# Optimization experiments

Hardware: AMD Instinct MI355X
Metric: run time of the kernel (lower is better)

The kernel has to match this reference:

```python
import jax, jax.numpy as jnp
import numpy as np

N = 4096   # number of observations
Q = 1024   # number of spatial locations (dist_matrix side)


def setup_inputs() -> dict:
    key = jax.random.key(0)
    k1, k2, k3, k4 = jax.random.split(key, 4)
    y_true = jax.random.normal(k1, (N, 1), dtype=jnp.float32)
    y_pred = jax.random.normal(k2, (N, 1), dtype=jnp.float32)
    Z_idx = jax.random.randint(k3, (N, 1), 0, Q).astype(jnp.int64)
    # symmetric distance matrix from random 2D coordinates
    coords = jax.random.uniform(k4, (Q, 2), dtype=jnp.float32) * 10.0
    diff = coords[:, None, :] - coords[None, :, :]
    dist_matrix = jnp.sqrt(jnp.sum(diff * diff, axis=-1) + 1e-12)
    sig2e = jnp.asarray(1.0, dtype=jnp.float32)
    sig2bs = jnp.ones((2,), dtype=jnp.float32)
    return {"y_true": y_true, "y_pred": y_pred, "Z_idx": Z_idx,
            "dist_matrix": dist_matrix, "sig2e": sig2e, "sig2bs": sig2bs}


def reference(y_true, y_pred, Z_idx, dist_matrix, sig2e, sig2bs):
    # NLL for the 'spatial' mixed-effects mode (custom_loss_lm).
    # V = sig2e*I + Z D Z^T with Z the one-hot indicator of Z_idx and
    # D[a,b] = sig2bs[0]*exp(-dist[a,b]/(2*sig2bs[1])).
    # Z D Z^T for one-hot Z is simply the row/col gather D[idx][:, idx],
    # which avoids materializing the dense N x Q indicator matrix.
    n = y_true.shape[0]
    idx = Z_idx[:, 0]
    D = sig2bs[0] * jnp.exp(-dist_matrix / (2.0 * sig2bs[1]))   # (Q, Q)
    V = sig2e * jnp.eye(n, dtype=jnp.float32) + D[idx][:, idx]  # (N, N)
    r = y_true - y_pred                                          # (N, 1)
    V_inv_r = jnp.linalg.solve(V, r)                             # (N, 1)
    quad = jnp.sum(r * V_inv_r)
    _, logdet = jnp.linalg.slogdet(V)
    log2pi = jnp.asarray(np.log(2.0 * np.pi), dtype=jnp.float32)
    total_loss = 0.5 * n * log2pi + 0.5 * logdet + 0.5 * quad
    return total_loss
```

## Files before the change

kernel.cpp:

```cpp
#include <hip/hip_runtime.h>
#include <math.h>

#define NN 4096
#define QQ 1024
#define LDA 1032
#define AF (1025 * 1032)


__device__ __forceinline__ void potrf64_run(float (&x)[16], int i, int q,
                                            float2 (&col2)[2][64]) {
#pragma unroll
    for (int qk = 0; qk < 4; ++qk) {
#pragma unroll
        for (int c2 = 0; c2 < 8; ++c2) {
            const int k = qk * 16 + 2 * c2;
            const int ck = 2 * c2;
            const int b = c2 & 1;
            if (q == qk) {
                float xk = x[ck];
                float d0 = __shfl(xk, k, 64);
                float rs0 = rsqrtf(d0);
                float l0 = (i == k) ? d0 * rs0 : xk * rs0;
                if (i >= k) x[ck] = l0;
                float lk1 = __shfl(l0, k + 1, 64);
                float x1v = fmaf(-l0, lk1, x[ck + 1]);
                float d1 = __shfl(x1v, k + 1, 64);
                float rs1 = rsqrtf(d1);
                float l1 = (i == k + 1) ? d1 * rs1 : x1v * rs1;
                if (i >= k + 1) x[ck + 1] = l1;
                col2[b][i] = make_float2(l0, l1);
            }
            __syncthreads();
            if (16 * q + 15 > k + 1 && i > k) {
                float2 lp = col2[b][i];
                const float4* cp = (const float4*)(&col2[b][16 * q]);
#pragma unroll
                for (int m2 = 0; m2 < 8; ++m2) {
                    float4 v = cp[m2];
                    if (16 * q + 2 * m2 > k + 1)
                        x[2 * m2] = fmaf(-lp.x, v.x, fmaf(-lp.y, v.y, x[2 * m2]));
                    if (16 * q + 2 * m2 + 1 > k + 1)
                        x[2 * m2 + 1] = fmaf(-lp.x, v.z, fmaf(-lp.y, v.w, x[2 * m2 + 1]));
                }
            }
        }
    }
}

template<int K, int M>
struct TAcc {
    static __device__ __forceinline__ void run(const float (&Lb)[64][65], const float (&x)[64],
                                               float& a0, float& a1) {
        if constexpr (M < K)     a0 = fmaf(-Lb[K][M], x[M], a0);
        if constexpr (M + 1 < K) a1 = fmaf(-Lb[K][M + 1], x[M + 1], a1);
        if constexpr (M + 2 < K) TAcc<K, M + 2>::run(Lb, x, a0, a1);
    }
};
template<int K>
struct TStep {
    static __device__ __forceinline__ void run(const float (&Lb)[64][65], const float (&dinv)[64],
                                               float (&x)[64]) {
        if constexpr (K < 64) {
            float a0 = x[K], a1 = 0.f;
            TAcc<K, 0>::run(Lb, x, a0, a1);
            x[K] = (a0 + a1) * dinv[K];
            TStep<K + 1>::run(Lb, dinv, x);
        }
    }
};

__device__ __forceinline__ void panel_tile(
    float* __restrict__ A, float* __restrict__ scal, int p, int by, int bx,
    int nr, int ncol, float (&PrRaw)[64 * 68], float (&PcRaw)[64 * 68],
    float2 (&col2)[2][64], float (&Lb)[64][65], float (&dinv)[64]) {
    const int tid = threadIdx.x;
    const int lane = tid & 63, wid = tid >> 6;
    int t0v = (p + 1) * 64;
    int r0 = t0v + by * 64;
    int c0 = t0v + bx * 64;
    bool wrow = (by == nr - 1);
    bool same_rc = (bx == by) && !wrow;
    bool dfuse = (bx == 0 && by == 0);
    int pc0 = p * 64;
    const float* db = A + (size_t)pc0 * (LDA + 1);
    for (int idx2 = tid; idx2 < 1024; idx2 += 256) {
        int rr = idx2 >> 4, c4 = idx2 & 15;
        int gr = r0 + rr;
        float4 v = make_float4(0.f, 0.f, 0.f, 0.f);
        if (gr <= QQ) v = *(const float4*)(A + (size_t)gr * LDA + pc0 + 4 * c4);
        *(float4*)(PrRaw + rr * 68 + 4 * c4) = v;
        if (!same_rc) {
            float4 u = *(const float4*)(A + (size_t)(c0 + rr) * LDA + pc0 + 4 * c4);
            *(float4*)(PcRaw + rr * 68 + 4 * c4) = u;
        }
    }
    for (int kk = tid; kk < 4096; kk += 256) {
        int ii = kk >> 6, jj = kk & 63;
        Lb[ii][jj] = db[(size_t)ii * LDA + jj];
    }
    if (tid < 64) dinv[tid] = 1.0f / db[(size_t)tid * (LDA + 1)];
    __syncthreads();
    if (wid == 0 && wrow) {
        float xv = PrRaw[lane];
        for (int k = 0; k < 64; ++k) {
            if (lane == k) xv *= dinv[k];
            float xk = __shfl(xv, k, 64);
            if (lane > k) xv = fmaf(-Lb[lane][k], xk, xv);
        }
        PrRaw[lane] = xv;
        if (bx == 0) {
            float v = xv * xv;
            for (int o = 32; o > 0; o >>= 1) v += __shfl_down(v, o, 64);
            if (lane == 0) atomicAdd(&scal[2], v);
        }
    } else {
        float* tp = nullptr;
        if (wid == 0) tp = PrRaw + lane * 68;
        else if (wid == 1 && !same_rc) tp = PcRaw + lane * 68;
        if (tp) {
            float x[64];
#pragma unroll
            for (int m = 0; m < 64; ++m) x[m] = tp[m];
            TStep<0>::run(Lb, dinv, x);
#pragma unroll
            for (int m = 0; m < 64; ++m) tp[m] = x[m];
        }
    }
    __syncthreads();
    const float* PB = same_rc ? PrRaw : PcRaw;
    int tx = tid & 15, ty = tid >> 4;
    float acc[4][4];
#pragma unroll
    for (int ii = 0; ii < 4; ++ii)
#pragma unroll
        for (int jj = 0; jj < 4; ++jj) acc[ii][jj] = 0.f;
    float4 ar4[4], br4[4];
#pragma unroll 4
    for (int k4 = 0; k4 < 16; ++k4) {
#pragma unroll
        for (int ii = 0; ii < 4; ++ii)
            ar4[ii] = *(const float4*)(PrRaw + (ty + 16 * ii) * 68 + 4 * k4);
#pragma unroll
        for (int jj = 0; jj < 4; ++jj)
            br4[jj] = *(const float4*)(PB + (tx + 16 * jj) * 68 + 4 * k4);
#pragma unroll
        for (int ii = 0; ii < 4; ++ii)
#pragma unroll
            for (int jj = 0; jj < 4; ++jj) {
                acc[ii][jj] = fmaf(ar4[ii].x, br4[jj].x, acc[ii][jj]);
                acc[ii][jj] = fmaf(ar4[ii].y, br4[jj].y, acc[ii][jj]);
                acc[ii][jj] = fmaf(ar4[ii].z, br4[jj].z, acc[ii][jj]);
                acc[ii][jj] = fmaf(ar4[ii].w, br4[jj].w, acc[ii][jj]);
            }
    }
    if (!dfuse) {
#pragma unroll
        for (int ii = 0; ii < 4; ++ii) {
            int rr = r0 + ty + 16 * ii;
            if (rr <= QQ) {
#pragma unroll
                for (int jj = 0; jj < 4; ++jj) {
                    float* pa = A + (size_t)rr * LDA + c0 + tx + 16 * jj;
                    *pa -= acc[ii][jj];
                }
            }
        }
    } else {
#pragma unroll
        for (int ii = 0; ii < 4; ++ii) {
            int lr = ty + 16 * ii;
#pragma unroll
            for (int jj = 0; jj < 4; ++jj) {
                int lc = tx + 16 * jj;
                float old = A[(size_t)(r0 + lr) * LDA + c0 + lc];
                PcRaw[lr * 65 + lc] = old - acc[ii][jj];
            }
        }
        __syncthreads();
        int i = tid & 63, q = tid >> 6;
        float x[16];
#pragma unroll
        for (int m = 0; m < 16; ++m) x[m] = PcRaw[i * 65 + 16 * q + m];
        potrf64_run(x, i, q, col2);
        float* row = A + (size_t)(r0 + i) * LDA + c0 + 16 * q;
#pragma unroll
        for (int m4 = 0; m4 < 4; ++m4)
            ((float4*)row)[m4] = make_float4(x[4 * m4], x[4 * m4 + 1],
                                             x[4 * m4 + 2], x[4 * m4 + 3]);
    }
}

__global__ __launch_bounds__(256) void k_front(
    const float* __restrict__ yt, const float* __restrict__ yp,
    const int* __restrict__ idx, const float* __restrict__ dist,
    const float* __restrict__ se_p, const float* __restrict__ sbs,
    float* __restrict__ A, float* __restrict__ scal) {
    const int bid = blockIdx.x, tid = threadIdx.x;
    const int lane = tid & 63, wid = tid >> 6;
    __shared__ int   c_l[1024];
    __shared__ float s_l[1024];
    __shared__ float sq_l[1024];
    __shared__ __align__(16) float Pc[64 * 65];
    __shared__ float2 col2[2][64];
    __shared__ float red[4];
    float sb0 = sbs[0];
    float inv2 = 1.0f / (2.0f * sbs[1]);
    float inv_se = 1.0f / se_p[0];
    bool mv = (bid >= 128);

    for (int j = tid; j < 1024; j += 256) { c_l[j] = 0; s_l[j] = 0.f; }
    __syncthreads();
    float rr_acc = 0.f;
#pragma unroll
    for (int e4 = 0; e4 < 16; ++e4) {
        int e = tid + 256 * e4;
        int q = idx[e];
        atomicAdd(&c_l[q], 1);
        if (mv) {
            float r = yt[e] - yp[e];
            atomicAdd(&s_l[q], r);
            rr_acc += r * r;
        }
    }
    __syncthreads();
    for (int j = tid; j < 1024; j += 256) sq_l[j] = sqrtf((float)c_l[j]);
    __syncthreads();

    if (bid == 0) {
        for (int kk = tid; kk < 4096; kk += 256) {
            int i = kk >> 6, j = kk & 63;
            float qi = sq_l[i] * inv_se * sb0;
            Pc[i * 65 + j] = ((i == j) ? 1.0f : 0.0f)
                           + qi * sq_l[j] * __expf(-dist[(size_t)i * QQ + j] * inv2);
        }
        __syncthreads();
        int i = lane, q = wid;
        float x[16];
#pragma unroll
        for (int m = 0; m < 16; ++m) x[m] = Pc[i * 65 + 16 * q + m];
        potrf64_run(x, i, q, col2);
        float* row = A + (size_t)i * LDA + 16 * q;
#pragma unroll
        for (int m4 = 0; m4 < 4; ++m4)
            ((float4*)row)[m4] = make_float4(x[4 * m4], x[4 * m4 + 1],
                                             x[4 * m4 + 2], x[4 * m4 + 3]);
        if (tid == 0) scal[2] = 0.f;
    } else if (!mv) {
        for (int i = 64 + (bid - 1); i < QQ; i += 127) {
            float qi = sq_l[i] * inv_se * sb0;
            float4 d = ((const float4*)(dist + (size_t)i * QQ))[tid];
            int j0 = 4 * tid;
            float4 o;
            o.x = ((i == j0    ) ? 1.0f : 0.0f) + qi * sq_l[j0    ] * __expf(-d.x * inv2);
            o.y = ((i == j0 + 1) ? 1.0f : 0.0f) + qi * sq_l[j0 + 1] * __expf(-d.y * inv2);
            o.z = ((i == j0 + 2) ? 1.0f : 0.0f) + qi * sq_l[j0 + 2] * __expf(-d.z * inv2);
            o.w = ((i == j0 + 3) ? 1.0f : 0.0f) + qi * sq_l[j0 + 3] * __expf(-d.w * inv2);
            ((float4*)(A + (size_t)i * LDA))[tid] = o;
        }
    } else {
        int m = bid - 128;
        if (bid == 128) {
            float v = rr_acc;
            for (int o = 32; o > 0; o >>= 1) v += __shfl_down(v, o, 64);
            if (lane == 0) red[wid] = v;
            __syncthreads();
            if (tid == 0) scal[0] = red[0] + red[1] + red[2] + red[3];
            __syncthreads();
        }
        float st_acc = 0.f;
#pragma unroll
        for (int h = 0; h < 2; ++h) {
            int row = m * 8 + wid * 2 + h;
            const float* dr = dist + (size_t)row * QQ;
            float acc = 0.f;
#pragma unroll
            for (int j4 = 0; j4 < 16; ++j4) {
                int j = lane + 64 * j4;
                acc += __expf(-dr[j] * inv2) * s_l[j];
            }
            for (int o = 32; o > 0; o >>= 1) acc += __shfl_down(acc, o, 64);
            if (lane == 0) {
                float tv = acc * sb0;
                A[(size_t)QQ * LDA + row] = sq_l[row] * tv;
                st_acc += s_l[row] * tv;
            }
        }
        __syncthreads();
        if (lane == 0) red[wid] = st_acc;
        __syncthreads();
        if (tid == 0) scal[16 + m] = red[0] + red[1] + red[2] + red[3];
    }
}

__global__ __launch_bounds__(256) void k_panel(float* __restrict__ A,
                                               float* __restrict__ scal, int p) {
    __shared__ __align__(16) float PrRaw[64 * 68];
    __shared__ __align__(16) float PcRaw[64 * 68];
    __shared__ float2 col2[2][64];
    __shared__ float Lb[64][65];
    __shared__ float dinv[64];
    int t0v = (p + 1) * 64;
    int rows = (QQ + 1) - t0v;
    int nr = (rows + 63) >> 6;
    int ncol = (QQ - t0v) / 64;
    int by = -1, bx = 0, rem = blockIdx.x;
    for (int b = 0; b < nr; ++b) {
        int cn = (b + 1 < ncol) ? (b + 1) : ncol;
        if (cn < 1) cn = 1;
        if (rem < cn) { by = b; bx = rem; break; }
        rem -= cn;
    }
    if (by < 0) return;
    panel_tile(A, scal, p, by, bx, nr, ncol, PrRaw, PcRaw, col2, Lb, dinv);
}

__global__ __launch_bounds__(256) void k_final(float* __restrict__ A,
                                               float* __restrict__ scal,
                                               const float* __restrict__ se_p,
                                               float* __restrict__ out) {
    const int tid = threadIdx.x;
    const int lane = tid & 63, wid = tid >> 6;
    __shared__ float Lb[64][65];
    __shared__ float r1s[4], r2s[4], r3s[4];
    __shared__ float wl[64];
    const float* db15 = A + (size_t)960 * LDA + 960;
    for (int kk = tid; kk < 4096; kk += 256) {
        int ii = kk >> 6, jj = kk & 63;
        Lb[ii][jj] = db15[(size_t)ii * LDA + jj];
    }
    __syncthreads();
    if (tid < 64) {
        float xv = A[(size_t)QQ * LDA + 960 + tid];
        for (int k = 0; k < 64; ++k) {
            if (tid == k) xv /= Lb[k][k];
            float xk = __shfl(xv, k, 64);
            if (tid > k) xv = fmaf(-Lb[tid][k], xk, xv);
        }
        wl[tid] = xv;
    }
    __syncthreads();
    float v1 = 0.f, v2 = 0.f;
    for (int i = tid; i < QQ; i += 256) {
        v1 += __logf(A[(size_t)i * LDA + i]);
        if (i >= 960) { float yv = wl[i - 960]; v2 += yv * yv; }
    }
    v1 *= 2.0f;
    float v3 = (tid < 128) ? scal[16 + tid] : 0.f;
    for (int o = 32; o > 0; o >>= 1) {
        v1 += __shfl_down(v1, o, 64);
        v2 += __shfl_down(v2, o, 64);
        v3 += __shfl_down(v3, o, 64);
    }
    if (lane == 0) { r1s[wid] = v1; r2s[wid] = v2; r3s[wid] = v3; }
    __syncthreads();
    if (tid == 0) {
        float ld = r1s[0] + r1s[1] + r1s[2] + r1s[3];
        float wsq = __hip_atomic_load(&scal[2], __ATOMIC_RELAXED, __HIP_MEMORY_SCOPE_AGENT);
        float yy = r2s[0] + r2s[1] + r2s[2] + r2s[3] + wsq;
        float st = r3s[0] + r3s[1] + r3s[2] + r3s[3];
        float se = se_p[0], inv = 1.0f / se;
        float rr = scal[0];
        float quad = rr * inv - inv * inv * (st - inv * yy);
        float logdetV = (float)NN * __logf(se) + ld;
        out[0] = 0.5f * (float)NN * 1.8378770664093453f + 0.5f * logdetV + 0.5f * quad;
    }
}

extern "C" void kernel_launch(void* const* d_in, const int* in_sizes, int n_in,
                              void* d_out, int out_size, void* d_ws, size_t ws_size,
                              hipStream_t stream) {
    const float* yt   = (const float*)d_in[0];
    const float* yp   = (const float*)d_in[1];
    const int*   idx  = (const int*)d_in[2];
    const float* dist = (const float*)d_in[3];
    const float* se   = (const float*)d_in[4];
    const float* sbs  = (const float*)d_in[5];
    float* out = (float*)d_out;

    float* W    = (float*)d_ws;
    float* A    = W;
    float* scal = W + AF;

    k_front<<<dim3(256), dim3(256), 0, stream>>>(yt, yp, idx, dist, se, sbs, A, scal);
    for (int p = 0; p <= 14; ++p) {
        int t0v = (p + 1) * 64;
        int nr = ((QQ + 1) - t0v + 63) / 64;
        int ncol = (QQ - t0v) / 64;
        int tiles = 0;
        for (int b = 0; b < nr; ++b) {
            int cn = (b + 1 < ncol) ? (b + 1) : ncol;
            if (cn < 1) cn = 1;
            tiles += cn;
        }
        k_panel<<<dim3(tiles), dim3(256), 0, stream>>>(A, scal, p);
    }
    k_final<<<dim3(1), dim3(256), 0, stream>>>(A, scal, se, out);
}
```

Baseline: 643.7 us.

## Parallelize panel triangular solve across all four waves with column-pair blocking

Replaces the per-lane serial 64-step forward substitution, where only one or two waves did all the work, with a cooperative TRSM. All 256 threads take part: each lane owns 16 columns of one row, and column pairs are broadcast through shared memory with a barrier per pair step. The special single-vector path for the last row is folded into the generic tile solve. The cost is 32 barriers per tile, and the Pr and Pc tiles are now solved one after the other instead of concurrently on separate waves.

```diff
diff --git a/kernel.cpp b/kernel.cpp
--- a/kernel.cpp
+++ b/kernel.cpp
@@ -47,27 +47,55 @@
     }
 }
 
-template<int K, int M>
-struct TAcc {
-    static __device__ __forceinline__ void run(const float (&Lb)[64][65], const float (&x)[64],
-                                               float& a0, float& a1) {
-        if constexpr (M < K)     a0 = fmaf(-Lb[K][M], x[M], a0);
-        if constexpr (M + 1 < K) a1 = fmaf(-Lb[K][M + 1], x[M + 1], a1);
-        if constexpr (M + 2 < K) TAcc<K, M + 2>::run(Lb, x, a0, a1);
-    }
-};
-template<int K>
-struct TStep {
-    static __device__ __forceinline__ void run(const float (&Lb)[64][65], const float (&dinv)[64],
-                                               float (&x)[64]) {
-        if constexpr (K < 64) {
-            float a0 = x[K], a1 = 0.f;
-            TAcc<K, 0>::run(Lb, x, a0, a1);
-            x[K] = (a0 + a1) * dinv[K];
-            TStep<K + 1>::run(Lb, dinv, x);
-        }
-    }
-};
+__device__ __forceinline__ void trsm64_tile(float* T, const float (&Lb)[64][65],
+                                            const float (&dinv)[64],
+                                            float2 (&col2)[2][64]) {
+    const int tid = threadIdx.x;
+    const int r = tid & 63, q = tid >> 6;
+    float* tp = T + r * 68 + 16 * q;
+    float x[16];
+#pragma unroll
+    for (int m4 = 0; m4 < 4; ++m4) {
+        float4 v = ((const float4*)tp)[m4];
+        x[4 * m4] = v.x; x[4 * m4 + 1] = v.y; x[4 * m4 + 2] = v.z; x[4 * m4 + 3] = v.w;
+    }
+#pragma unroll
+    for (int qk = 0; qk < 4; ++qk) {
+#pragma unroll
+        for (int c2 = 0; c2 < 8; ++c2) {
+            const int k = qk * 16 + 2 * c2;
+            const int ck = 2 * c2;
+            const int b = c2 & 1;
+            if (q == qk) {
+                float l0 = x[ck] * dinv[k];
+                x[ck] = l0;
+                float x1 = fmaf(-l0, Lb[k + 1][k], x[ck + 1]);
+                float l1 = x1 * dinv[k + 1];
+                x[ck + 1] = l1;
+                col2[b][r] = make_float2(l0, l1);
+            }
+            __syncthreads();
+            if (16 * q + 15 > k + 1) {
+                float2 lp = col2[b][r];
+#pragma unroll
+                for (int m2 = 0; m2 < 8; ++m2) {
+                    const int c0 = 16 * q + 2 * m2;
+                    if (c0 > k + 1)
+                        x[2 * m2] = fmaf(-lp.x, Lb[c0][k],
+                                         fmaf(-lp.y, Lb[c0][k + 1], x[2 * m2]));
+                    if (c0 + 1 > k + 1)
+                        x[2 * m2 + 1] = fmaf(-lp.x, Lb[c0 + 1][k],
+                                             fmaf(-lp.y, Lb[c0 + 1][k + 1], x[2 * m2 + 1]));
+                }
+            }
+        }
+    }
+#pragma unroll
+    for (int m4 = 0; m4 < 4; ++m4)
+        ((float4*)tp)[m4] = make_float4(x[4 * m4], x[4 * m4 + 1],
+                                        x[4 * m4 + 2], x[4 * m4 + 3]);
+    __syncthreads();
+}
 
 __device__ __forceinline__ void panel_tile(
     float* __restrict__ A, float* __restrict__ scal, int p, int by, int bx,
@@ -100,33 +128,14 @@
     }
     if (tid < 64) dinv[tid] = 1.0f / db[(size_t)tid * (LDA + 1)];
     __syncthreads();
-    if (wid == 0 && wrow) {
+    trsm64_tile(PrRaw, Lb, dinv, col2);
+    if (!same_rc) trsm64_tile(PcRaw, Lb, dinv, col2);
+    if (wrow && bx == 0 && wid == 0) {
         float xv = PrRaw[lane];
-        for (int k = 0; k < 64; ++k) {
-            if (lane == k) xv *= dinv[k];
-            float xk = __shfl(xv, k, 64);
-            if (lane > k) xv = fmaf(-Lb[lane][k], xk, xv);
-        }
-        PrRaw[lane] = xv;
-        if (bx == 0) {
-            float v = xv * xv;
-            for (int o = 32; o > 0; o >>= 1) v += __shfl_down(v, o, 64);
-            if (lane == 0) atomicAdd(&scal[2], v);
-        }
-    } else {
-        float* tp = nullptr;
-        if (wid == 0) tp = PrRaw + lane * 68;
-        else if (wid == 1 && !same_rc) tp = PcRaw + lane * 68;
-        if (tp) {
-            float x[64];
-#pragma unroll
-            for (int m = 0; m < 64; ++m) x[m] = tp[m];
-            TStep<0>::run(Lb, dinv, x);
-#pragma unroll
-            for (int m = 0; m < 64; ++m) tp[m] = x[m];
-        }
-    }
-    __syncthreads();
+        float v = xv * xv;
+        for (int o = 32; o > 0; o >>= 1) v += __shfl_down(v, o, 64);
+        if (lane == 0) atomicAdd(&scal[2], v);
+    }
     const float* PB = same_rc ? PrRaw : PcRaw;
     int tx = tid & 15, ty = tid >> 4;
     float acc[4][4];
```

Result: slower. 872.9 us (+35.6%).
